# Kernel optimization log

Measured on AMD Instinct MI355X. Metric: run time of the kernel, lower is better.

## Reference

```python
import jax, jax.numpy as jnp
import numpy as np

HID = 1024
BATCH = 32
SRC_LEN = 2048


def setup_inputs() -> dict:
    key = jax.random.key(0)
    k1, k2, k3, k4, k5 = jax.random.split(key, 5)
    hidden = jax.random.normal(k1, (BATCH, HID), dtype=jnp.float32)
    encoder_outputs = jax.random.normal(k2, (SRC_LEN, BATCH, 2 * HID), dtype=jnp.float32)
    # nn.Linear(3*hid, hid): weight [hid, 3*hid], bias [hid]
    lim_a = 1.0 / np.sqrt(3 * HID)
    attn_w = jax.random.uniform(k3, (HID, 3 * HID), minval=-lim_a, maxval=lim_a, dtype=jnp.float32)
    attn_b = jax.random.uniform(k4, (HID,), minval=-lim_a, maxval=lim_a, dtype=jnp.float32)
    # nn.Linear(hid, 1, bias=False): weight [1, hid] -> store as [hid]
    lim_v = 1.0 / np.sqrt(HID)
    v_w = jax.random.uniform(k5, (HID,), minval=-lim_v, maxval=lim_v, dtype=jnp.float32)
    return {"hidden": hidden, "encoder_outputs": encoder_outputs,
            "attn_w": attn_w, "attn_b": attn_b, "v_w": v_w}


def reference(hidden, encoder_outputs, attn_w, attn_b, v_w):
    # hidden: [B, H]; encoder_outputs: [S, B, 2H]
    enc = jnp.transpose(encoder_outputs, (1, 0, 2))  # [B, S, 2H]
    # Split the concat-Linear: cat([hidden, enc]) @ W^T == hidden @ Wh^T + enc @ We^T
    w_h = attn_w[:, :HID]          # [H, H]   acts on repeated hidden
    w_e = attn_w[:, HID:]          # [H, 2H]  acts on encoder outputs
    h_proj = hidden @ w_h.T        # [B, H]
    e_proj = jnp.einsum('bse,he->bsh', enc, w_e)  # [B, S, H]
    energy = jnp.tanh(h_proj[:, None, :] + e_proj + attn_b)  # [B, S, H]
    attention = jnp.einsum('bsh,h->bs', energy, v_w)          # [B, S]
    return jax.nn.softmax(attention, axis=1)
```

## Files before the change

### kernel.cpp

```cpp
#include <hip/hip_runtime.h>
#include <hip/hip_bf16.h>
#include <stdint.h>

#define HID   1024
#define KD    2048
#define NK    (KD/64)
#define BATCH 32
#define SRC   2048

typedef __attribute__((ext_vector_type(4))) float  f32x4;
typedef __attribute__((ext_vector_type(8))) __bf16 bf16x8;
typedef __attribute__((ext_vector_type(4))) __bf16 bf16x4;

__global__ __launch_bounds__(256) void prep_w_kernel(const float* __restrict__ attn_w,
                                                     __bf16* __restrict__ wbuf,
                                                     float* __restrict__ out)
{
    int gid = blockIdx.x * 256 + threadIdx.x;
    int p = gid << 2;
    int h = p >> 11;
    int e = p & 2047;
    f32x4 w = *(const f32x4*)(attn_w + (size_t)h * 3072 + HID + e);
    bf16x4 o = { (__bf16)w[0], (__bf16)w[1], (__bf16)w[2], (__bf16)w[3] };
    *(bf16x4*)(wbuf + p) = o;
    if (gid < 16384) {
        f32x4 z = {0.f, 0.f, 0.f, 0.f};
        ((f32x4*)out)[gid] = z;
    }
}

__global__ __launch_bounds__(256) void prep_h_kernel(const float* __restrict__ hidden,
                                                     const float* __restrict__ attn_w,
                                                     const float* __restrict__ attn_b,
                                                     float* __restrict__ hb)
{
    int gid = blockIdx.x * 256 + threadIdx.x;
    int b = gid & 31;
    int h = gid >> 5;
    const float* hp = hidden + b * HID;
    const float* wp = attn_w + (size_t)h * 3072;
    float acc = 0.f;
    #pragma unroll 4
    for (int k = 0; k < HID; k += 4) {
        f32x4 hv = *(const f32x4*)(hp + k);
        f32x4 wv = *(const f32x4*)(wp + k);
        acc += hv[0]*wv[0] + hv[1]*wv[1] + hv[2]*wv[2] + hv[3]*wv[3];
    }
    hb[b * HID + h] = acc + attn_b[h];
}

__global__ __launch_bounds__(256, 2)
void fused_attn_gemm(const float* __restrict__ enc,
                     const __bf16* __restrict__ wb,
                     const float* __restrict__ hb,
                     const float* __restrict__ v_w,
                     float* __restrict__ out)
{
    const int bid = blockIdx.x;
    const int mt  = bid >> 3;
    const int nc  = bid & 7;
    const int m0  = mt * 128;
    const int h0  = nc * 128;

    const int tid  = threadIdx.x;
    const int wid  = tid >> 6;
    const int lane = tid & 63;
    const int wr   = wid >> 1;
    const int wc   = wid & 1;
    const int l15  = lane & 15;
    const int g    = lane >> 4;

    __shared__ __attribute__((aligned(16))) __bf16 lA[2][128 * 64];
    __shared__ __attribute__((aligned(16))) __bf16 lB[2][128 * 64];

    f32x4 acc[4][4];
    #pragma unroll
    for (int i = 0; i < 4; ++i)
        #pragma unroll
        for (int j = 0; j < 4; ++j)
            acc[i][j] = (f32x4){0.f, 0.f, 0.f, 0.f};

    const int ar = tid >> 1;
    const int ah = tid & 1;
    const float* aBase = enc + (size_t)(m0 + ar) * KD + ah * 32;
    const int aswz = ar & 7;

    int bofs[4];
    const __bf16* bsrc[4];
    #pragma unroll
    for (int i = 0; i < 4; ++i) {
        int o  = (i * 256 + tid) * 16;
        int r  = o >> 7;
        int pc = (o >> 4) & 7;
        int c  = pc ^ (r & 7);
        bofs[i] = o >> 1;
        bsrc[i] = wb + (size_t)(h0 + r) * KD + c * 8;
    }

    int rA[4], rB[4];
    #pragma unroll
    for (int i = 0; i < 4; ++i) {
        rA[i] = (wr * 64 + i * 16 + l15) * 64;
        rB[i] = (wc * 64 + i * 16 + l15) * 64;
    }
    const int sw0 = ((0 + g) ^ (l15 & 7)) * 8;
    const int sw1 = ((4 + g) ^ (l15 & 7)) * 8;

    f32x4 sreg[8];

    auto loadA = [&](int kt) {
        #pragma unroll
        for (int q = 0; q < 8; ++q)
            sreg[q] = *(const f32x4*)(aBase + kt * 64 + q * 4);
    };
    auto writeA = [&](int buf) {
        #pragma unroll
        for (int q = 0; q < 4; ++q) {
            f32x4 x = sreg[2*q], y = sreg[2*q+1];
            bf16x8 v = { (__bf16)x[0], (__bf16)x[1], (__bf16)x[2], (__bf16)x[3],
                         (__bf16)y[0], (__bf16)y[1], (__bf16)y[2], (__bf16)y[3] };
            int pc = (ah * 4 + q) ^ aswz;
            *(bf16x8*)&lA[buf][ar * 64 + pc * 8] = v;
        }
    };
    auto issueB = [&](int buf, int kt) {
        #pragma unroll
        for (int i = 0; i < 4; ++i) {
            __builtin_amdgcn_global_load_lds(
                (const __attribute__((address_space(1))) void*)(bsrc[i] + kt * 64),
                (__attribute__((address_space(3))) void*)&lB[buf][bofs[i]],
                16, 0, 0);
        }
    };
    auto compute = [&](int buf) {
        #pragma unroll
        for (int ks = 0; ks < 2; ++ks) {
            const int sw = ks ? sw1 : sw0;
            bf16x8 af[4], bfv[4];
            #pragma unroll
            for (int i = 0; i < 4; ++i) af[i]  = *(const bf16x8*)&lA[buf][rA[i] + sw];
            #pragma unroll
            for (int i = 0; i < 4; ++i) bfv[i] = *(const bf16x8*)&lB[buf][rB[i] + sw];
            #pragma unroll
            for (int mi = 0; mi < 4; ++mi)
                #pragma unroll
                for (int ni = 0; ni < 4; ++ni)
                    acc[mi][ni] = __builtin_amdgcn_mfma_f32_16x16x32_bf16(
                        af[mi], bfv[ni], acc[mi][ni], 0, 0, 0);
        }
    };

    loadA(0);
    issueB(0, 0);
    writeA(0);
    __syncthreads();

    for (int kt = 0; kt < NK; ++kt) {
        const int cur = kt & 1;
        if (kt + 1 < NK) { loadA(kt + 1); issueB(cur ^ 1, kt + 1); }
        compute(cur);
        if (kt + 1 < NK) writeA(cur ^ 1);
        __syncthreads();
    }

    float vw[4];
    #pragma unroll
    for (int ni = 0; ni < 4; ++ni)
        vw[ni] = v_w[h0 + wc * 64 + ni * 16 + l15];

    #pragma unroll
    for (int mi = 0; mi < 4; ++mi) {
        #pragma unroll
        for (int j = 0; j < 4; ++j) {
            const int m = m0 + wr * 64 + mi * 16 + g * 4 + j;
            const int b = m & 31;
            const int s = m >> 5;
            const float* hbrow = hb + b * HID + h0 + wc * 64;
            float sum = 0.f;
            #pragma unroll
            for (int ni = 0; ni < 4; ++ni) {
                float e = acc[mi][ni][j] + hbrow[ni * 16 + l15];
                sum += tanhf(e) * vw[ni];
            }
            sum += __shfl_xor(sum, 1);
            sum += __shfl_xor(sum, 2);
            sum += __shfl_xor(sum, 4);
            sum += __shfl_xor(sum, 8);
            if (l15 == 0)
                atomicAdd(&out[b * SRC + s], sum);
        }
    }
}

__global__ __launch_bounds__(256) void softmax_kernel(float* __restrict__ out)
{
    const int b = blockIdx.x;
    const int t = threadIdx.x;
    const int wid = t >> 6, lane = t & 63;
    __shared__ float redm[4], reds[4];

    float v[8];
    float mx = -3.4e38f;
    #pragma unroll
    for (int i = 0; i < 8; ++i) {
        v[i] = out[b * SRC + i * 256 + t];
        mx = fmaxf(mx, v[i]);
    }
    #pragma unroll
    for (int o = 1; o < 64; o <<= 1) mx = fmaxf(mx, __shfl_xor(mx, o));
    if (lane == 0) redm[wid] = mx;
    __syncthreads();
    mx = fmaxf(fmaxf(redm[0], redm[1]), fmaxf(redm[2], redm[3]));

    float sum = 0.f;
    #pragma unroll
    for (int i = 0; i < 8; ++i) { v[i] = expf(v[i] - mx); sum += v[i]; }
    #pragma unroll
    for (int o = 1; o < 64; o <<= 1) sum += __shfl_xor(sum, o);
    if (lane == 0) reds[wid] = sum;
    __syncthreads();
    sum = reds[0] + reds[1] + reds[2] + reds[3];

    const float inv = 1.f / sum;
    #pragma unroll
    for (int i = 0; i < 8; ++i) out[b * SRC + i * 256 + t] = v[i] * inv;
}

extern "C" void kernel_launch(void* const* d_in, const int* in_sizes, int n_in,
                              void* d_out, int out_size, void* d_ws, size_t ws_size,
                              hipStream_t stream)
{
    const float* hidden = (const float*)d_in[0];
    const float* enc    = (const float*)d_in[1];
    const float* attn_w = (const float*)d_in[2];
    const float* attn_b = (const float*)d_in[3];
    const float* v_w    = (const float*)d_in[4];
    float* out = (float*)d_out;

    __bf16* wbuf = (__bf16*)d_ws;
    float*  hb   = (float*)((char*)d_ws + (size_t)(4u << 20));

    prep_w_kernel<<<2048, 256, 0, stream>>>(attn_w, wbuf, out);
    prep_h_kernel<<<128, 256, 0, stream>>>(hidden, attn_w, attn_b, hb);
    fused_attn_gemm<<<4096, 256, 0, stream>>>(enc, wbuf, hb, v_w, out);
    softmax_kernel<<<32, 256, 0, stream>>>(out);
}
```

Baseline: 1.469 ms.

## Load A operand directly from global into MFMA registers, drop A LDS staging

The GEMM kernel stops staging the fp32 encoder tile through LDS and instead has each lane load and convert its own A fragments straight from global memory inside the compute loop. Only B is still double-buffered in LDS, which halves LDS use and allows occupancy to be raised to 3 blocks per CU. The block index is remapped so blocks sharing an encoder tile run concurrently, and each N-chunk starts its K loop at a staggered offset to spread cache and channel pressure. The prep_h kernel also splits the K reduction across four lanes for more parallelism. The risk is that A loads now sit exposed in the MFMA loop without software prefetch, and each A tile is read once per N-chunk straight from global or L2.

```diff
diff --git a/kernel.cpp b/kernel.cpp
--- a/kernel.cpp
+++ b/kernel.cpp
@@ -35,21 +35,24 @@
                                                      float* __restrict__ hb)
 {
     int gid = blockIdx.x * 256 + threadIdx.x;
-    int b = gid & 31;
-    int h = gid >> 5;
-    const float* hp = hidden + b * HID;
-    const float* wp = attn_w + (size_t)h * 3072;
+    int kc = gid & 3;
+    int b  = (gid >> 2) & 31;
+    int h  = gid >> 7;
+    const float* hp = hidden + b * HID + kc * 256;
+    const float* wp = attn_w + (size_t)h * 3072 + kc * 256;
     float acc = 0.f;
-    #pragma unroll 4
-    for (int k = 0; k < HID; k += 4) {
+    #pragma unroll 8
+    for (int k = 0; k < 256; k += 4) {
         f32x4 hv = *(const f32x4*)(hp + k);
         f32x4 wv = *(const f32x4*)(wp + k);
         acc += hv[0]*wv[0] + hv[1]*wv[1] + hv[2]*wv[2] + hv[3]*wv[3];
     }
-    hb[b * HID + h] = acc + attn_b[h];
-}
-
-__global__ __launch_bounds__(256, 2)
+    acc += __shfl_xor(acc, 1);
+    acc += __shfl_xor(acc, 2);
+    if (kc == 0) hb[b * HID + h] = acc + attn_b[h];
+}
+
+__global__ __launch_bounds__(256, 3)
 void fused_attn_gemm(const float* __restrict__ enc,
                      const __bf16* __restrict__ wb,
                      const float* __restrict__ hb,
@@ -57,10 +60,13 @@
                      float* __restrict__ out)
 {
     const int bid = blockIdx.x;
-    const int mt  = bid >> 3;
-    const int nc  = bid & 7;
+    const int x   = bid & 7;
+    const int j   = bid >> 3;
+    const int mt  = x * 64 + (j >> 3);
+    const int nc  = j & 7;
     const int m0  = mt * 128;
     const int h0  = nc * 128;
+    const int kt0 = nc * 4;
 
     const int tid  = threadIdx.x;
     const int wid  = tid >> 6;
@@ -70,20 +76,14 @@
     const int l15  = lane & 15;
     const int g    = lane >> 4;
 
-    __shared__ __attribute__((aligned(16))) __bf16 lA[2][128 * 64];
     __shared__ __attribute__((aligned(16))) __bf16 lB[2][128 * 64];
 
     f32x4 acc[4][4];
     #pragma unroll
     for (int i = 0; i < 4; ++i)
         #pragma unroll
-        for (int j = 0; j < 4; ++j)
-            acc[i][j] = (f32x4){0.f, 0.f, 0.f, 0.f};
-
-    const int ar = tid >> 1;
-    const int ah = tid & 1;
-    const float* aBase = enc + (size_t)(m0 + ar) * KD + ah * 32;
-    const int aswz = ar & 7;
+        for (int jj = 0; jj < 4; ++jj)
+            acc[i][jj] = (f32x4){0.f, 0.f, 0.f, 0.f};
 
     int bofs[4];
     const __bf16* bsrc[4];
@@ -97,32 +97,18 @@
         bsrc[i] = wb + (size_t)(h0 + r) * KD + c * 8;
     }
 
-    int rA[4], rB[4];
-    #pragma unroll
-    for (int i = 0; i < 4; ++i) {
-        rA[i] = (wr * 64 + i * 16 + l15) * 64;
+    int rB[4];
+    #pragma unroll
+    for (int i = 0; i < 4; ++i)
         rB[i] = (wc * 64 + i * 16 + l15) * 64;
-    }
     const int sw0 = ((0 + g) ^ (l15 & 7)) * 8;
     const int sw1 = ((4 + g) ^ (l15 & 7)) * 8;
 
-    f32x4 sreg[8];
-
-    auto loadA = [&](int kt) {
-        #pragma unroll
-        for (int q = 0; q < 8; ++q)
-            sreg[q] = *(const f32x4*)(aBase + kt * 64 + q * 4);
-    };
-    auto writeA = [&](int buf) {
-        #pragma unroll
-        for (int q = 0; q < 4; ++q) {
-            f32x4 x = sreg[2*q], y = sreg[2*q+1];
-            bf16x8 v = { (__bf16)x[0], (__bf16)x[1], (__bf16)x[2], (__bf16)x[3],
-                         (__bf16)y[0], (__bf16)y[1], (__bf16)y[2], (__bf16)y[3] };
-            int pc = (ah * 4 + q) ^ aswz;
-            *(bf16x8*)&lA[buf][ar * 64 + pc * 8] = v;
-        }
-    };
+    const float* aRow[4];
+    #pragma unroll
+    for (int i = 0; i < 4; ++i)
+        aRow[i] = enc + (size_t)(m0 + wr * 64 + i * 16 + l15) * KD + g * 8;
+
     auto issueB = [&](int buf, int kt) {
         #pragma unroll
         for (int i = 0; i < 4; ++i) {
@@ -132,15 +118,22 @@
                 16, 0, 0);
         }
     };
-    auto compute = [&](int buf) {
+    auto compute = [&](int buf, int kt) {
         #pragma unroll
         for (int ks = 0; ks < 2; ++ks) {
             const int sw = ks ? sw1 : sw0;
-            bf16x8 af[4], bfv[4];
-            #pragma unroll
-            for (int i = 0; i < 4; ++i) af[i]  = *(const bf16x8*)&lA[buf][rA[i] + sw];
+            bf16x8 bfv[4];
             #pragma unroll
             for (int i = 0; i < 4; ++i) bfv[i] = *(const bf16x8*)&lB[buf][rB[i] + sw];
+            bf16x8 af[4];
+            #pragma unroll
+            for (int mi = 0; mi < 4; ++mi) {
+                const float* a0 = aRow[mi] + kt * 64 + ks * 32;
+                f32x4 xv = *(const f32x4*)a0;
+                f32x4 yv = *(const f32x4*)(a0 + 4);
+                af[mi] = (bf16x8){ (__bf16)xv[0], (__bf16)xv[1], (__bf16)xv[2], (__bf16)xv[3],
+                                   (__bf16)yv[0], (__bf16)yv[1], (__bf16)yv[2], (__bf16)yv[3] };
+            }
             #pragma unroll
             for (int mi = 0; mi < 4; ++mi)
                 #pragma unroll
@@ -150,16 +143,14 @@
         }
     };
 
-    loadA(0);
-    issueB(0, 0);
-    writeA(0);
+    issueB(0, kt0);
     __syncthreads();
 
-    for (int kt = 0; kt < NK; ++kt) {
-        const int cur = kt & 1;
-        if (kt + 1 < NK) { loadA(kt + 1); issueB(cur ^ 1, kt + 1); }
-        compute(cur);
-        if (kt + 1 < NK) writeA(cur ^ 1);
+    for (int t = 0; t < NK; ++t) {
+        const int cur = t & 1;
+        const int kt  = (kt0 + t) & (NK - 1);
+        if (t + 1 < NK) issueB(cur ^ 1, (kt0 + t + 1) & (NK - 1));
+        compute(cur, kt);
         __syncthreads();
     }
 
@@ -171,15 +162,15 @@
     #pragma unroll
     for (int mi = 0; mi < 4; ++mi) {
         #pragma unroll
-        for (int j = 0; j < 4; ++j) {
-            const int m = m0 + wr * 64 + mi * 16 + g * 4 + j;
+        for (int jj = 0; jj < 4; ++jj) {
+            const int m = m0 + wr * 64 + mi * 16 + g * 4 + jj;
             const int b = m & 31;
             const int s = m >> 5;
             const float* hbrow = hb + b * HID + h0 + wc * 64;
             float sum = 0.f;
             #pragma unroll
             for (int ni = 0; ni < 4; ++ni) {
-                float e = acc[mi][ni][j] + hbrow[ni * 16 + l15];
+                float e = acc[mi][ni][jj] + hbrow[ni * 16 + l15];
                 sum += tanhf(e) * vw[ni];
             }
             sum += __shfl_xor(sum, 1);
@@ -241,7 +232,7 @@
     float*  hb   = (float*)((char*)d_ws + (size_t)(4u << 20));
 
     prep_w_kernel<<<2048, 256, 0, stream>>>(attn_w, wbuf, out);
-    prep_h_kernel<<<128, 256, 0, stream>>>(hidden, attn_w, attn_b, hb);
+    prep_h_kernel<<<512, 256, 0, stream>>>(hidden, attn_w, attn_b, hb);
     fused_attn_gemm<<<4096, 256, 0, stream>>>(enc, wbuf, hb, v_w, out);
     softmax_kernel<<<32, 256, 0, stream>>>(out);
 }
```

Measured after the change: 1.632 ms. 1.11x slower.
